# Optimization experiments

Hardware: AMD Instinct MI355X
Metric: run time of the kernel (lower is better)

## Reference

```python
import jax, jax.numpy as jnp
import numpy as np

B, N, M, C, H = 4, 2048, 2048, 1024, 16
D = C // H  # head_dim = 64
SCALE = D ** -0.5


def setup_inputs() -> dict:
    key = jax.random.key(0)
    ks = jax.random.split(key, 8)
    std = C ** -0.5
    return {
        "query": jax.random.normal(ks[0], (B, N, C), jnp.float32),
        "key": jax.random.normal(ks[1], (B, M, C), jnp.float32),
        "value": jax.random.normal(ks[2], (B, M, C), jnp.float32),
        "Wq": jax.random.normal(ks[3], (C, C), jnp.float32) * std,
        "Wk": jax.random.normal(ks[4], (C, C), jnp.float32) * std,
        "Wv": jax.random.normal(ks[5], (C, C), jnp.float32) * std,
        "Wp": jax.random.normal(ks[6], (C, C), jnp.float32) * std,
        "bp": jax.random.normal(ks[7], (C,), jnp.float32) * 0.01,
    }


def reference(query, key, value, Wq, Wk, Wv, Wp, bp):
    # Linear: y = x @ W.T (torch nn.Linear convention), no bias for q/k/v.
    # reshape (B,S,C)->(B,S,H,D)->(B,H,S,D)
    q = jnp.einsum('bnc,dc->bnd', query, Wq).reshape(B, N, H, D).transpose(0, 2, 1, 3)
    k = jnp.einsum('bmc,dc->bmd', key, Wk).reshape(B, M, H, D).transpose(0, 2, 1, 3)
    v = jnp.einsum('bmc,dc->bmd', value, Wv).reshape(B, M, H, D).transpose(0, 2, 1, 3)
    # scaled scores, softmax over keys
    attn = jnp.einsum('bhnd,bhmd->bhnm', q * SCALE, k)
    attn = jax.nn.softmax(attn, axis=-1)
    # attention output -> (B,N,C)
    x = jnp.einsum('bhnm,bhmd->bhnd', attn, v).transpose(0, 2, 1, 3).reshape(B, N, C)
    # output projection with bias
    return jnp.einsum('bnc,dc->bnd', x, Wp) + bp
```

## Files before the change

### kernel.cpp

```cpp
#include <hip/hip_runtime.h>
#include <stdint.h>

#define B_ 4
#define N_ 2048
#define M_ 2048
#define C_ 1024
#define H_ 16
#define D_ 64
#define SC_ (B_*N_*C_)
#define CC_ (C_*C_)

typedef unsigned short u16;
typedef __attribute__((ext_vector_type(8))) short short8;
typedef __attribute__((ext_vector_type(4))) short short4v;
typedef __attribute__((ext_vector_type(4))) float f32x4;

#if __has_builtin(__builtin_amdgcn_exp2f)
#define EXP2F __builtin_amdgcn_exp2f
#else
#define EXP2F exp2f
#endif

__device__ inline u16 f2bf(float f) {
    union { float f; uint32_t u; } v; v.f = f;
    uint32_t r = v.u + 0x7fffu + ((v.u >> 16) & 1u);
    return (u16)(r >> 16);
}

__device__ inline f32x4 mfma16x16x16_bf16(short4v a, short4v b, f32x4 c) {
#if __has_builtin(__builtin_amdgcn_mfma_f32_16x16x16bf16_1k)
    return __builtin_amdgcn_mfma_f32_16x16x16bf16_1k(a, b, c, 0, 0, 0);
#else
    asm volatile("v_mfma_f32_16x16x16_bf16 %0, %1, %2, %0"
                 : "+v"(c) : "v"(a), "v"(b));
    return c;
#endif
}

#define WAIT_BARRIER(N)                                         \
    do {                                                        \
        asm volatile("s_waitcnt vmcnt(" #N ")" ::: "memory");   \
        __builtin_amdgcn_s_barrier();                           \
        __builtin_amdgcn_sched_barrier(0);                      \
    } while (0)

__global__ __launch_bounds__(256) void convert_kernel(
    const float* __restrict__ q, const float* __restrict__ k, const float* __restrict__ v,
    const float* __restrict__ wq, const float* __restrict__ wk,
    const float* __restrict__ wv, const float* __restrict__ wp,
    u16* __restrict__ qf, u16* __restrict__ kf, u16* __restrict__ vf,
    u16* __restrict__ wqb, u16* __restrict__ wkb, u16* __restrict__ wvb, u16* __restrict__ wpb)
{
    const int SC4 = SC_ / 4;
    const int CC4 = CC_ / 4;
    const int total = 3 * SC4 + 4 * CC4;
    for (int i = blockIdx.x * 256 + threadIdx.x; i < total; i += gridDim.x * 256) {
        const float* src; u16* dst; int off;
        if (i < 3 * SC4) {
            int seg = i >> 21;
            off = (i & (SC4 - 1)) << 2;
            src = seg == 0 ? q : seg == 1 ? k : v;
            dst = seg == 0 ? qf : seg == 1 ? kf : vf;
        } else {
            int j = i - 3 * SC4;
            int seg = j >> 18;
            off = (j & (CC4 - 1)) << 2;
            src = seg == 0 ? wq : seg == 1 ? wk : seg == 2 ? wv : wp;
            dst = seg == 0 ? wqb : seg == 1 ? wkb : seg == 2 ? wvb : wpb;
        }
        float4 val = *(const float4*)(src + off);
        ushort4 h;
        h.x = f2bf(val.x); h.y = f2bf(val.y); h.z = f2bf(val.z); h.w = f2bf(val.w);
        *(ushort4*)(dst + off) = h;
    }
}

template<int OMODE>
__global__ __launch_bounds__(256) void gemm_lds(
    const u16* __restrict__ A, const u16* __restrict__ Wb,
    const float* __restrict__ bias, void* __restrict__ Op, float scale)
{
    const int K = 1024;
    __shared__ u16 SH[3 * 8192];
    const int tid = threadIdx.x;
    const int wid = tid >> 6, lane = tid & 63;
    const int quad = lane >> 4, l15 = lane & 15;
    const int f = blockIdx.x;
    const int m0 = (f & 63) * 128, n0 = (f >> 6) * 128;
    const int wm = (wid >> 1) * 64, wn = (wid & 1) * 64;

    size_t aoff[2], boff[2];
    int dsto[2];
#pragma unroll
    for (int i = 0; i < 2; ++i) {
        int s = tid + i * 256;
        int row = s >> 2, c8 = (s & 3) << 3;
        aoff[i] = (size_t)(m0 + row) * K + c8;
        boff[i] = (size_t)(n0 + row) * K + c8;
        dsto[i] = s * 8;
    }

    f32x4 acc[4][4];
#pragma unroll
    for (int i = 0; i < 4; ++i)
#pragma unroll
        for (int j = 0; j < 4; ++j) acc[i][j] = f32x4{0.f, 0.f, 0.f, 0.f};

#pragma unroll
    for (int t = 0; t < 2; ++t) {
        const int bo = t * 8192, k0 = t * 32;
#pragma unroll
        for (int i = 0; i < 2; ++i) {
            __builtin_amdgcn_global_load_lds(
                (const __attribute__((address_space(1))) void*)(A + aoff[i] + k0),
                (__attribute__((address_space(3))) void*)(SH + bo + dsto[i]), 16, 0, 0);
            __builtin_amdgcn_global_load_lds(
                (const __attribute__((address_space(1))) void*)(Wb + boff[i] + k0),
                (__attribute__((address_space(3))) void*)(SH + bo + 4096 + dsto[i]), 16, 0, 0);
        }
    }

    for (int it = 0; it < 32; ++it) {
        const int cur = (it % 3) * 8192;
        if (it < 31) WAIT_BARRIER(4);
        else         WAIT_BARRIER(0);
        if (it + 2 < 32) {
            const int nxt = ((it + 2) % 3) * 8192;
            const int k0n = (it + 2) * 32;
#pragma unroll
            for (int i = 0; i < 2; ++i) {
                __builtin_amdgcn_global_load_lds(
                    (const __attribute__((address_space(1))) void*)(A + aoff[i] + k0n),
                    (__attribute__((address_space(3))) void*)(SH + nxt + dsto[i]), 16, 0, 0);
                __builtin_amdgcn_global_load_lds(
                    (const __attribute__((address_space(1))) void*)(Wb + boff[i] + k0n),
                    (__attribute__((address_space(3))) void*)(SH + nxt + 4096 + dsto[i]), 16, 0, 0);
            }
        }
        short8 av[4], bv[4];
#pragma unroll
        for (int i = 0; i < 4; ++i)
            av[i] = *(const short8*)(SH + cur + (wm + i * 16 + l15) * 32 + quad * 8);
#pragma unroll
        for (int j = 0; j < 4; ++j)
            bv[j] = *(const short8*)(SH + cur + 4096 + (wn + j * 16 + l15) * 32 + quad * 8);
#pragma unroll
        for (int i = 0; i < 4; ++i)
#pragma unroll
            for (int j = 0; j < 4; ++j)
                acc[i][j] = __builtin_amdgcn_mfma_f32_16x16x32_bf16(av[i], bv[j], acc[i][j], 0, 0, 0);
    }

    if (OMODE == 2) {
#pragma unroll
        for (int j = 0; j < 4; ++j) {
            int col = n0 + wn + j * 16 + l15;
            float bb = bias[col];
#pragma unroll
            for (int i = 0; i < 4; ++i) {
                int row = m0 + wm + i * 16 + quad * 4;
#pragma unroll
                for (int r = 0; r < 4; ++r)
                    ((float*)Op)[(size_t)(row + r) * 1024 + col] = acc[i][j][r] * scale + bb;
            }
        }
    } else if (OMODE == 0) {
#pragma unroll
        for (int j = 0; j < 4; ++j) {
            int col = n0 + wn + j * 16 + l15;
#pragma unroll
            for (int i = 0; i < 4; ++i) {
                int row = m0 + wm + i * 16 + quad * 4;
#pragma unroll
                for (int r = 0; r < 4; ++r)
                    ((u16*)Op)[(size_t)(row + r) * 1024 + col] = f2bf(acc[i][j][r] * scale);
            }
        }
    } else {
#pragma unroll
        for (int j = 0; j < 4; ++j) {
            int col = n0 + wn + j * 16 + l15;
            int hh = col >> 6, dd = col & 63;
#pragma unroll
            for (int i = 0; i < 4; ++i) {
                int row = m0 + wm + i * 16 + quad * 4;
                int bb = row >> 11, mm = row & 2047;
                ushort4 hv;
                hv.x = f2bf(acc[i][j][0] * scale);
                hv.y = f2bf(acc[i][j][1] * scale);
                hv.z = f2bf(acc[i][j][2] * scale);
                hv.w = f2bf(acc[i][j][3] * scale);
                *(ushort4*)((u16*)Op + (((size_t)bb * 16 + hh) * 64 + dd) * 2048 + mm) = hv;
            }
        }
    }
}

__global__ __launch_bounds__(256, 3) void attn_kernel(
    const u16* __restrict__ qg, const u16* __restrict__ kg,
    const u16* __restrict__ vT, u16* __restrict__ xb)
{
    __shared__ __align__(16) char smem[49152];
    u16* KV = (u16*)smem;
    float* Ored = (float*)smem;
    float* Lred = (float*)(smem + 16384);

    const int tid = threadIdx.x;
    const int wid = tid >> 6, lane = tid & 63;
    const int quad = lane >> 4, l15 = lane & 15;
    const int f = blockIdx.x;
    const int bh = f & 63, qt = f >> 6;
    const int b = bh >> 4, h = bh & 15;

    const u16* qbase = qg + ((size_t)(b * N_ + qt * 64)) * C_ + h * 64;
    short8 qf[4][2];
#pragma unroll
    for (int qb2 = 0; qb2 < 4; ++qb2)
#pragma unroll
        for (int ch = 0; ch < 2; ++ch)
            qf[qb2][ch] = *(const short8*)(qbase + (size_t)(qb2 * 16 + l15) * C_ + ch * 32 + quad * 8);

    const u16* kptr[2];
    const u16* vptr[2];
    int dsto[2];
#pragma unroll
    for (int i = 0; i < 2; ++i) {
        int s = tid + i * 256;
        int row = s >> 3, g = s & 7;
        int gsw = g ^ (row & 7);
        kptr[i] = kg + ((size_t)(b * M_ + row)) * C_ + h * 64 + gsw * 8;
        vptr[i] = vT + (((size_t)b * 16 + h) * 64 + row) * M_ + gsw * 8;
        dsto[i] = s * 8;
    }

    f32x4 acc_o[4][4];
#pragma unroll
    for (int i = 0; i < 4; ++i)
#pragma unroll
        for (int j = 0; j < 4; ++j) acc_o[i][j] = f32x4{0.f, 0.f, 0.f, 0.f};
    float lsum[4] = {0.f, 0.f, 0.f, 0.f};

    const int rk = wid * 16 + l15, swk = rk & 7;
    const int kfo0 = rk * 64 + ((0 * 4 + quad) ^ swk) * 8;
    const int kfo1 = rk * 64 + ((1 * 4 + quad) ^ swk) * 8;
    int vfo[4];
#pragma unroll
    for (int db = 0; db < 4; ++db) {
        int rv = db * 16 + l15, swv = rv & 7;
        vfo[db] = 4096 + rv * 64 + (((wid * 2 + (quad >> 1)) ^ swv) << 3) + ((quad & 1) << 2);
    }

    union { short4v s; uint32_t u[2]; } pfrag[4], vfu;

#pragma unroll
    for (int t = 0; t < 2; ++t) {
        const int bo = t * 8192, kv0 = t * 64;
#pragma unroll
        for (int i = 0; i < 2; ++i) {
            __builtin_amdgcn_global_load_lds(
                (const __attribute__((address_space(1))) void*)(kptr[i] + (size_t)kv0 * C_),
                (__attribute__((address_space(3))) void*)(KV + bo + dsto[i]), 16, 0, 0);
            __builtin_amdgcn_global_load_lds(
                (const __attribute__((address_space(1))) void*)(vptr[i] + kv0),
                (__attribute__((address_space(3))) void*)(KV + bo + 4096 + dsto[i]), 16, 0, 0);
        }
    }

    for (int it = 0; it < 32; ++it) {
        const int cur = (it % 3) * 8192;
        if (it < 31) WAIT_BARRIER(4);
        else         WAIT_BARRIER(0);
        if (it + 2 < 32) {
            const int nxt = ((it + 2) % 3) * 8192;
            const int kvn = (it + 2) * 64;
#pragma unroll
            for (int i = 0; i < 2; ++i) {
                __builtin_amdgcn_global_load_lds(
                    (const __attribute__((address_space(1))) void*)(kptr[i] + (size_t)kvn * C_),
                    (__attribute__((address_space(3))) void*)(KV + nxt + dsto[i]), 16, 0, 0);
                __builtin_amdgcn_global_load_lds(
                    (const __attribute__((address_space(1))) void*)(vptr[i] + kvn),
                    (__attribute__((address_space(3))) void*)(KV + nxt + 4096 + dsto[i]), 16, 0, 0);
            }
        }

        short8 kf0 = *(const short8*)(KV + cur + kfo0);
        short8 kf1 = *(const short8*)(KV + cur + kfo1);
        f32x4 sc[4];
#pragma unroll
        for (int qb2 = 0; qb2 < 4; ++qb2) {
            sc[qb2] = f32x4{0.f, 0.f, 0.f, 0.f};
            sc[qb2] = __builtin_amdgcn_mfma_f32_16x16x32_bf16(kf0, qf[qb2][0], sc[qb2], 0, 0, 0);
            sc[qb2] = __builtin_amdgcn_mfma_f32_16x16x32_bf16(kf1, qf[qb2][1], sc[qb2], 0, 0, 0);
        }

#pragma unroll
        for (int qb2 = 0; qb2 < 4; ++qb2) {
            float e0 = EXP2F(sc[qb2][0]);
            float e1 = EXP2F(sc[qb2][1]);
            float e2 = EXP2F(sc[qb2][2]);
            float e3 = EXP2F(sc[qb2][3]);
            lsum[qb2] += (e0 + e1) + (e2 + e3);
            pfrag[qb2].u[0] = __builtin_amdgcn_perm(__builtin_bit_cast(uint32_t, e1),
                                                    __builtin_bit_cast(uint32_t, e0), 0x07060302u);
            pfrag[qb2].u[1] = __builtin_amdgcn_perm(__builtin_bit_cast(uint32_t, e3),
                                                    __builtin_bit_cast(uint32_t, e2), 0x07060302u);
        }

#pragma unroll
        for (int db = 0; db < 4; ++db) {
            uint2 vlo = *(const uint2*)(KV + cur + vfo[db]);
            vfu.u[0] = vlo.x; vfu.u[1] = vlo.y;
#pragma unroll
            for (int qb2 = 0; qb2 < 4; ++qb2)
                acc_o[qb2][db] = mfma16x16x16_bf16(vfu.s, pfrag[qb2].s, acc_o[qb2][db]);
        }
    }

    __syncthreads();
    *(f32x4*)(Lred + (((wid * 4 + quad) * 16 + l15) << 2)) =
        f32x4{lsum[0], lsum[1], lsum[2], lsum[3]};
    __syncthreads();
    float dsum = 0.f;
#pragma unroll
    for (int q2 = 0; q2 < 4; ++q2)
        dsum += Lred[(((quad * 4 + q2) * 16 + l15) << 2) + wid];
    dsum += __shfl_xor(dsum, 16);
    dsum += __shfl_xor(dsum, 32);
    float dinv = 1.f / dsum;

#pragma unroll
    for (int qb2 = 0; qb2 < 4; ++qb2) {
        __syncthreads();
#pragma unroll
        for (int db = 0; db < 4; ++db)
            *(f32x4*)(Ored + (((wid * 4 + db) * 64 + lane) << 2)) = acc_o[qb2][db];
        __syncthreads();
        if (wid == qb2) {
#pragma unroll
            for (int w2 = 0; w2 < 4; ++w2) {
                if (w2 == wid) continue;
#pragma unroll
                for (int db = 0; db < 4; ++db) {
                    f32x4 t = *(const f32x4*)(Ored + (((w2 * 4 + db) * 64 + lane) << 2));
                    acc_o[qb2][db] += t;
                }
            }
            size_t ob = ((size_t)(b * N_ + qt * 64 + wid * 16 + l15)) * C_ + h * 64;
#pragma unroll
            for (int db = 0; db < 4; ++db) {
                ushort4 st;
                st.x = f2bf(acc_o[qb2][db][0] * dinv);
                st.y = f2bf(acc_o[qb2][db][1] * dinv);
                st.z = f2bf(acc_o[qb2][db][2] * dinv);
                st.w = f2bf(acc_o[qb2][db][3] * dinv);
                *(ushort4*)(xb + ob + db * 16 + quad * 4) = st;
            }
        }
    }
}

extern "C" void kernel_launch(void* const* d_in, const int* in_sizes, int n_in,
                              void* d_out, int out_size, void* d_ws, size_t ws_size,
                              hipStream_t stream) {
    const float* query = (const float*)d_in[0];
    const float* key   = (const float*)d_in[1];
    const float* value = (const float*)d_in[2];
    const float* Wq    = (const float*)d_in[3];
    const float* Wk    = (const float*)d_in[4];
    const float* Wv    = (const float*)d_in[5];
    const float* Wpm   = (const float*)d_in[6];
    const float* bp    = (const float*)d_in[7];
    float* out = (float*)d_out;

    u16* base = (u16*)d_ws;
    u16* qf  = base;
    u16* kf  = base + (size_t)SC_;
    u16* vf  = base + (size_t)2 * SC_;
    u16* kb  = base + (size_t)3 * SC_;
    u16* Wqb = base + (size_t)4 * SC_;
    u16* Wkb = Wqb + CC_;
    u16* Wvb = Wkb + CC_;
    u16* Wpb = Wvb + CC_;
    u16* vTp = kf;
    u16* qb  = vf;
    u16* xb  = qf;

    hipLaunchKernelGGL(convert_kernel, dim3(4096), dim3(256), 0, stream,
                       query, key, value, Wq, Wk, Wv, Wpm,
                       qf, kf, vf, Wqb, Wkb, Wvb, Wpb);

    dim3 gg(512), bb(256);
    hipLaunchKernelGGL((gemm_lds<0>), gg, bb, 0, stream, kf, Wkb, nullptr, (void*)kb, 1.0f);
    hipLaunchKernelGGL((gemm_lds<1>), gg, bb, 0, stream, vf, Wvb, nullptr, (void*)vTp, 1.0f);
    hipLaunchKernelGGL((gemm_lds<0>), gg, bb, 0, stream, qf, Wqb, nullptr, (void*)qb,
                       0.125f * 1.44269504088896340736f);

    hipLaunchKernelGGL(attn_kernel, dim3(2048), bb, 0, stream, qb, kb, vTp, xb);

    hipLaunchKernelGGL((gemm_lds<2>), gg, bb, 0, stream, xb, Wpb, bp, (void*)out, 1.0f);
}
```

Before: 339.9 us.

## Split attention work by query rows per wave instead of by keys

Each wave now owns 32 query rows and iterates over all 64 keys of every KV tile, instead of the four waves splitting the keys and reducing partial outputs through shared memory. The block tile grows to 128 queries, so the grid halves, K/V tiles are reused across twice as many queries, and the end-of-kernel LDS reduction with its many barriers goes away. The KV pipeline also drops from triple buffering with counted waits to double buffering with a plain __syncthreads, which may expose more load latency.

```diff
diff --git a/kernel.cpp b/kernel.cpp
--- a/kernel.cpp
+++ b/kernel.cpp
@@ -200,10 +200,7 @@
     const u16* __restrict__ qg, const u16* __restrict__ kg,
     const u16* __restrict__ vT, u16* __restrict__ xb)
 {
-    __shared__ __align__(16) char smem[49152];
-    u16* KV = (u16*)smem;
-    float* Ored = (float*)smem;
-    float* Lred = (float*)(smem + 16384);
+    __shared__ __align__(16) u16 KV[2 * 8192];
 
     const int tid = threadIdx.x;
     const int wid = tid >> 6, lane = tid & 63;
@@ -212,10 +209,10 @@
     const int bh = f & 63, qt = f >> 6;
     const int b = bh >> 4, h = bh & 15;
 
-    const u16* qbase = qg + ((size_t)(b * N_ + qt * 64)) * C_ + h * 64;
-    short8 qf[4][2];
-#pragma unroll
-    for (int qb2 = 0; qb2 < 4; ++qb2)
+    const u16* qbase = qg + ((size_t)(b * N_ + qt * 128 + wid * 32)) * C_ + h * 64;
+    short8 qf[2][2];
+#pragma unroll
+    for (int qb2 = 0; qb2 < 2; ++qb2)
 #pragma unroll
         for (int ch = 0; ch < 2; ++ch)
             qf[qb2][ch] = *(const short8*)(qbase + (size_t)(qb2 * 16 + l15) * C_ + ch * 32 + quad * 8);
@@ -233,46 +230,43 @@
         dsto[i] = s * 8;
     }
 
-    f32x4 acc_o[4][4];
+    f32x4 acc[4][2];
 #pragma unroll
     for (int i = 0; i < 4; ++i)
 #pragma unroll
-        for (int j = 0; j < 4; ++j) acc_o[i][j] = f32x4{0.f, 0.f, 0.f, 0.f};
-    float lsum[4] = {0.f, 0.f, 0.f, 0.f};
-
-    const int rk = wid * 16 + l15, swk = rk & 7;
-    const int kfo0 = rk * 64 + ((0 * 4 + quad) ^ swk) * 8;
-    const int kfo1 = rk * 64 + ((1 * 4 + quad) ^ swk) * 8;
-    int vfo[4];
-#pragma unroll
-    for (int db = 0; db < 4; ++db) {
-        int rv = db * 16 + l15, swv = rv & 7;
-        vfo[db] = 4096 + rv * 64 + (((wid * 2 + (quad >> 1)) ^ swv) << 3) + ((quad & 1) << 2);
-    }
-
-    union { short4v s; uint32_t u[2]; } pfrag[4], vfu;
-
-#pragma unroll
-    for (int t = 0; t < 2; ++t) {
-        const int bo = t * 8192, kv0 = t * 64;
-#pragma unroll
-        for (int i = 0; i < 2; ++i) {
-            __builtin_amdgcn_global_load_lds(
-                (const __attribute__((address_space(1))) void*)(kptr[i] + (size_t)kv0 * C_),
-                (__attribute__((address_space(3))) void*)(KV + bo + dsto[i]), 16, 0, 0);
-            __builtin_amdgcn_global_load_lds(
-                (const __attribute__((address_space(1))) void*)(vptr[i] + kv0),
-                (__attribute__((address_space(3))) void*)(KV + bo + 4096 + dsto[i]), 16, 0, 0);
-        }
+        for (int j = 0; j < 2; ++j) acc[i][j] = f32x4{0.f, 0.f, 0.f, 0.f};
+    float lsum[2] = {0.f, 0.f};
+
+    const int swr = l15 & 7;
+    const int kxo0 = ((0 * 4 + quad) ^ swr) << 3;
+    const int kxo1 = ((1 * 4 + quad) ^ swr) << 3;
+    int vbase[4];
+#pragma unroll
+    for (int db = 0; db < 4; ++db)
+        vbase[db] = 4096 + (db * 16 + l15) * 64 + ((quad & 1) << 2);
+    int vx[4];
+#pragma unroll
+    for (int kt = 0; kt < 4; ++kt)
+        vx[kt] = ((kt * 2 + (quad >> 1)) ^ swr) << 3;
+
+    union { short4v s; uint32_t u[2]; } pfrag[2], vfu;
+
+#pragma unroll
+    for (int i = 0; i < 2; ++i) {
+        __builtin_amdgcn_global_load_lds(
+            (const __attribute__((address_space(1))) void*)(kptr[i]),
+            (__attribute__((address_space(3))) void*)(KV + dsto[i]), 16, 0, 0);
+        __builtin_amdgcn_global_load_lds(
+            (const __attribute__((address_space(1))) void*)(vptr[i]),
+            (__attribute__((address_space(3))) void*)(KV + 4096 + dsto[i]), 16, 0, 0);
     }
 
     for (int it = 0; it < 32; ++it) {
-        const int cur = (it % 3) * 8192;
-        if (it < 31) WAIT_BARRIER(4);
-        else         WAIT_BARRIER(0);
-        if (it + 2 < 32) {
-            const int nxt = ((it + 2) % 3) * 8192;
-            const int kvn = (it + 2) * 64;
+        const int cur = (it & 1) * 8192;
+        __syncthreads();
+        if (it + 1 < 32) {
+            const int nxt = ((it + 1) & 1) * 8192;
+            const int kvn = (it + 1) * 64;
 #pragma unroll
             for (int i = 0; i < 2; ++i) {
                 __builtin_amdgcn_global_load_lds(
@@ -284,78 +278,59 @@
             }
         }
 
-        short8 kf0 = *(const short8*)(KV + cur + kfo0);
-        short8 kf1 = *(const short8*)(KV + cur + kfo1);
-        f32x4 sc[4];
-#pragma unroll
-        for (int qb2 = 0; qb2 < 4; ++qb2) {
-            sc[qb2] = f32x4{0.f, 0.f, 0.f, 0.f};
-            sc[qb2] = __builtin_amdgcn_mfma_f32_16x16x32_bf16(kf0, qf[qb2][0], sc[qb2], 0, 0, 0);
-            sc[qb2] = __builtin_amdgcn_mfma_f32_16x16x32_bf16(kf1, qf[qb2][1], sc[qb2], 0, 0, 0);
-        }
-
-#pragma unroll
-        for (int qb2 = 0; qb2 < 4; ++qb2) {
-            float e0 = EXP2F(sc[qb2][0]);
-            float e1 = EXP2F(sc[qb2][1]);
-            float e2 = EXP2F(sc[qb2][2]);
-            float e3 = EXP2F(sc[qb2][3]);
-            lsum[qb2] += (e0 + e1) + (e2 + e3);
-            pfrag[qb2].u[0] = __builtin_amdgcn_perm(__builtin_bit_cast(uint32_t, e1),
-                                                    __builtin_bit_cast(uint32_t, e0), 0x07060302u);
-            pfrag[qb2].u[1] = __builtin_amdgcn_perm(__builtin_bit_cast(uint32_t, e3),
-                                                    __builtin_bit_cast(uint32_t, e2), 0x07060302u);
-        }
-
+#pragma unroll
+        for (int kt = 0; kt < 4; ++kt) {
+            const int kbase = cur + (kt * 16 + l15) * 64;
+            short8 kf0 = *(const short8*)(KV + kbase + kxo0);
+            short8 kf1 = *(const short8*)(KV + kbase + kxo1);
+            f32x4 sc0 = f32x4{0.f, 0.f, 0.f, 0.f};
+            f32x4 sc1 = f32x4{0.f, 0.f, 0.f, 0.f};
+            sc0 = __builtin_amdgcn_mfma_f32_16x16x32_bf16(kf0, qf[0][0], sc0, 0, 0, 0);
+            sc1 = __builtin_amdgcn_mfma_f32_16x16x32_bf16(kf0, qf[1][0], sc1, 0, 0, 0);
+            sc0 = __builtin_amdgcn_mfma_f32_16x16x32_bf16(kf1, qf[0][1], sc0, 0, 0, 0);
+            sc1 = __builtin_amdgcn_mfma_f32_16x16x32_bf16(kf1, qf[1][1], sc1, 0, 0, 0);
+
+#pragma unroll
+            for (int qb2 = 0; qb2 < 2; ++qb2) {
+                const f32x4 sv = qb2 ? sc1 : sc0;
+                float e0 = EXP2F(sv[0]);
+                float e1 = EXP2F(sv[1]);
+                float e2 = EXP2F(sv[2]);
+                float e3 = EXP2F(sv[3]);
+                lsum[qb2] += (e0 + e1) + (e2 + e3);
+                pfrag[qb2].u[0] = __builtin_amdgcn_perm(__builtin_bit_cast(uint32_t, e1),
+                                                        __builtin_bit_cast(uint32_t, e0), 0x07060302u);
+                pfrag[qb2].u[1] = __builtin_amdgcn_perm(__builtin_bit_cast(uint32_t, e3),
+                                                        __builtin_bit_cast(uint32_t, e2), 0x07060302u);
+            }
+
+#pragma unroll
+            for (int db = 0; db < 4; ++db) {
+                uint2 vlo = *(const uint2*)(KV + cur + vbase[db] + vx[kt]);
+                vfu.u[0] = vlo.x; vfu.u[1] = vlo.y;
+                acc[db][0] = mfma16x16x16_bf16(vfu.s, pfrag[0].s, acc[db][0]);
+                acc[db][1] = mfma16x16x16_bf16(vfu.s, pfrag[1].s, acc[db][1]);
+            }
+        }
+    }
+
+    lsum[0] += __shfl_xor(lsum[0], 16);
+    lsum[0] += __shfl_xor(lsum[0], 32);
+    lsum[1] += __shfl_xor(lsum[1], 16);
+    lsum[1] += __shfl_xor(lsum[1], 32);
+    const float dinv[2] = {1.f / lsum[0], 1.f / lsum[1]};
+
+#pragma unroll
+    for (int qb2 = 0; qb2 < 2; ++qb2) {
+        size_t ob = ((size_t)(b * N_ + qt * 128 + wid * 32 + qb2 * 16 + l15)) * C_ + h * 64;
 #pragma unroll
         for (int db = 0; db < 4; ++db) {
-            uint2 vlo = *(const uint2*)(KV + cur + vfo[db]);
-            vfu.u[0] = vlo.x; vfu.u[1] = vlo.y;
-#pragma unroll
-            for (int qb2 = 0; qb2 < 4; ++qb2)
-                acc_o[qb2][db] = mfma16x16x16_bf16(vfu.s, pfrag[qb2].s, acc_o[qb2][db]);
-        }
-    }
-
-    __syncthreads();
-    *(f32x4*)(Lred + (((wid * 4 + quad) * 16 + l15) << 2)) =
-        f32x4{lsum[0], lsum[1], lsum[2], lsum[3]};
-    __syncthreads();
-    float dsum = 0.f;
-#pragma unroll
-    for (int q2 = 0; q2 < 4; ++q2)
-        dsum += Lred[(((quad * 4 + q2) * 16 + l15) << 2) + wid];
-    dsum += __shfl_xor(dsum, 16);
-    dsum += __shfl_xor(dsum, 32);
-    float dinv = 1.f / dsum;
-
-#pragma unroll
-    for (int qb2 = 0; qb2 < 4; ++qb2) {
-        __syncthreads();
-#pragma unroll
-        for (int db = 0; db < 4; ++db)
-            *(f32x4*)(Ored + (((wid * 4 + db) * 64 + lane) << 2)) = acc_o[qb2][db];
-        __syncthreads();
-        if (wid == qb2) {
-#pragma unroll
-            for (int w2 = 0; w2 < 4; ++w2) {
-                if (w2 == wid) continue;
-#pragma unroll
-                for (int db = 0; db < 4; ++db) {
-                    f32x4 t = *(const f32x4*)(Ored + (((w2 * 4 + db) * 64 + lane) << 2));
-                    acc_o[qb2][db] += t;
-                }
-            }
-            size_t ob = ((size_t)(b * N_ + qt * 64 + wid * 16 + l15)) * C_ + h * 64;
-#pragma unroll
-            for (int db = 0; db < 4; ++db) {
-                ushort4 st;
-                st.x = f2bf(acc_o[qb2][db][0] * dinv);
-                st.y = f2bf(acc_o[qb2][db][1] * dinv);
-                st.z = f2bf(acc_o[qb2][db][2] * dinv);
-                st.w = f2bf(acc_o[qb2][db][3] * dinv);
-                *(ushort4*)(xb + ob + db * 16 + quad * 4) = st;
-            }
+            ushort4 st;
+            st.x = f2bf(acc[db][qb2][0] * dinv[qb2]);
+            st.y = f2bf(acc[db][qb2][1] * dinv[qb2]);
+            st.z = f2bf(acc[db][qb2][2] * dinv[qb2]);
+            st.w = f2bf(acc[db][qb2][3] * dinv[qb2]);
+            *(ushort4*)(xb + ob + db * 16 + quad * 4) = st;
         }
     }
 }
@@ -396,7 +371,7 @@
     hipLaunchKernelGGL((gemm_lds<0>), gg, bb, 0, stream, qf, Wqb, nullptr, (void*)qb,
                        0.125f * 1.44269504088896340736f);
 
-    hipLaunchKernelGGL(attn_kernel, dim3(2048), bb, 0, stream, qb, kb, vTp, xb);
+    hipLaunchKernelGGL(attn_kernel, dim3(1024), bb, 0, stream, qb, kb, vTp, xb);
 
     hipLaunchKernelGGL((gemm_lds<2>), gg, bb, 0, stream, xb, Wpb, bp, (void*)out, 1.0f);
 }
```

After: 344.5 us. No clear change (+1.3%).
